# Kernel optimization log

Hardware: AMD Instinct MI355X
Metric: run time of the kernel (lower is better)

Reference implementation:

```python
import jax, jax.numpy as jnp
import numpy as np
import math

D_MODEL = 768
NUM_HEADS = 12
D_K = D_MODEL // NUM_HEADS

def setup_inputs() -> dict:
    key = jax.random.key(0)
    k_x, k_q, k_k, k_v, k_o = jax.random.split(key, 5)
    x = jax.random.normal(k_x, (2, 2048, D_MODEL), dtype=jnp.float32)
    std = math.sqrt(2.0 / (D_MODEL + D_MODEL))
    # trunc_normal approx: clip normal to [-3std, 3std]
    def tn(k):
        return jnp.clip(jax.random.normal(k, (D_MODEL, D_MODEL), dtype=jnp.float32) * std, -3 * std, 3 * std)
    return {
        "x": x,
        "weight_query": tn(k_q),
        "weight_key": tn(k_k),
        "weight_value": tn(k_v),
        "weight_output": tn(k_o),
    }

def reference(x, weight_query, weight_key, weight_value, weight_output):
    # x: (b, s, d_model); weights: (d_out, d_model)
    b, s, _ = x.shape
    def proj_heads(w):
        y = jnp.einsum('od,bsd->bso', w, x)  # (b, s, h*dk)
        return y.reshape(b, s, NUM_HEADS, D_K).transpose(0, 2, 1, 3)  # (b, h, s, dk)
    Q = proj_heads(weight_query)
    K = proj_heads(weight_key)
    V = proj_heads(weight_value)
    scores = jnp.einsum('bhqd,bhkd->bhqk', Q, K) / jnp.sqrt(jnp.asarray(D_K, x.dtype))
    causal = jnp.tril(jnp.ones((s, s), dtype=bool))  # (sq, sk)
    scores = jnp.where(causal, scores, -jnp.inf)
    attn = jax.nn.softmax(scores, axis=-1)
    out_heads = jnp.einsum('bhqk,bhkd->bhqd', attn, V)  # (b, h, s, dv)
    attn_out = out_heads.transpose(0, 2, 1, 3).reshape(b, s, NUM_HEADS * D_K)
    return jnp.einsum('di,bsi->bsd', weight_output, attn_out)
```

## Files before the change

### kernel.cpp

```cpp
#include <hip/hip_runtime.h>
#include <stdint.h>

typedef float f32x4 __attribute__((ext_vector_type(4)));
typedef __bf16 bf16x8 __attribute__((ext_vector_type(8)));
typedef uint32_t u32a  __attribute__((may_alias));
typedef uint2    u2a   __attribute__((may_alias));
typedef uint4    u4a   __attribute__((may_alias));

#define VS 2064

__device__ __forceinline__ ushort f2b(float f) {
  uint32_t u = __builtin_bit_cast(uint32_t, f);
  u += 0x7FFFu + ((u >> 16) & 1u);
  return (ushort)(u >> 16);
}
__device__ __forceinline__ uint32_t b16(uint32_t u) {
  u += 0x7FFFu + ((u >> 16) & 1u);
  return u >> 16;
}
__device__ __forceinline__ float blo(uint32_t a) {
  return __builtin_bit_cast(float, a << 16);
}
__device__ __forceinline__ float bhi(uint32_t a) {
  return __builtin_bit_cast(float, a & 0xFFFF0000u);
}

__device__ __forceinline__ bf16x8 ld_frag(const ushort* p) {
  u4a u = *(const u4a*)p;
  return __builtin_bit_cast(bf16x8, u);
}

__device__ __forceinline__ u4a cvt8(const float* p) {
  u4a a = *(const u4a*)p, b = *(const u4a*)(p + 4), o;
  o.x = b16(a.x) | (b16(a.y) << 16);
  o.y = b16(a.z) | (b16(a.w) << 16);
  o.z = b16(b.x) | (b16(b.y) << 16);
  o.w = b16(b.z) | (b16(b.w) << 16);
  return o;
}

__device__ __forceinline__ void load_lds16(const void* g, void* l) {
  __builtin_amdgcn_global_load_lds(
      (const __attribute__((address_space(1))) uint32_t*)g,
      (__attribute__((address_space(3))) uint32_t*)l, 16, 0, 0);
}

__global__ __launch_bounds__(256) void convert_kernel(
    const float* __restrict__ x,  const float* __restrict__ wq,
    const float* __restrict__ wk, const float* __restrict__ wv,
    const float* __restrict__ wo,
    ushort* __restrict__ xb,  ushort* __restrict__ wqb,
    ushort* __restrict__ wkb, ushort* __restrict__ wvb,
    ushort* __restrict__ wob)
{
  const size_t NX = 3145728, NW = 589824;
  size_t idx = ((size_t)blockIdx.x * 256 + threadIdx.x) * 8;
  const float* src; ushort* dst; size_t off;
  if      (idx < NX)          { src = x;  dst = xb;  off = idx; }
  else if (idx < NX + NW)     { src = wq; dst = wqb; off = idx - NX; }
  else if (idx < NX + 2 * NW) { src = wk; dst = wkb; off = idx - NX - NW; }
  else if (idx < NX + 3 * NW) { src = wv; dst = wvb; off = idx - NX - 2 * NW; }
  else                        { src = wo; dst = wob; off = idx - NX - 3 * NW; }
  *(u4a*)(dst + off) = cvt8(src + off);
}

__global__ __launch_bounds__(256) void gemm_qkv(
    const ushort* __restrict__ A,
    const ushort* __restrict__ B0, const ushort* __restrict__ B1,
    const ushort* __restrict__ B2,
    ushort* __restrict__ Qo, ushort* __restrict__ Ko, ushort* __restrict__ Vt,
    int M, int N, int K)
{
  const ushort* B = blockIdx.z == 0 ? B0 : (blockIdx.z == 1 ? B1 : B2);
  const int m0 = blockIdx.x * 128, n0 = blockIdx.y * 64;
  __shared__ ushort As[128 * 64];
  __shared__ ushort Bs[64 * 64];
  const int tid = threadIdx.x, wave = tid >> 6, lane = tid & 63;
  const int quad = lane >> 4, l16 = lane & 15;
  const int mw = (wave & 1) * 64, nw = (wave >> 1) * 32;
  f32x4 acc[4][2] = {};

  for (int k0 = 0; k0 < K; k0 += 64) {
#pragma unroll
    for (int i = 0; i < 4; ++i) {
      int c = i * 256 + tid;
      load_lds16(A + (size_t)(m0 + (c >> 3)) * K + k0 + (c & 7) * 8,
                 As + (size_t)(i * 256 + wave * 64) * 8);
    }
#pragma unroll
    for (int i = 0; i < 2; ++i) {
      int c = i * 256 + tid;
      load_lds16(B + (size_t)(n0 + (c >> 3)) * K + k0 + (c & 7) * 8,
                 Bs + (size_t)(i * 256 + wave * 64) * 8);
    }
    __syncthreads();
#pragma unroll
    for (int ks = 0; ks < 2; ++ks) {
      bf16x8 af[4], bfr[2];
#pragma unroll
      for (int i = 0; i < 4; ++i)
        af[i]  = ld_frag(As + (mw + i * 16 + l16) * 64 + ks * 32 + quad * 8);
#pragma unroll
      for (int j = 0; j < 2; ++j)
        bfr[j] = ld_frag(Bs + (nw + j * 16 + l16) * 64 + ks * 32 + quad * 8);
#pragma unroll
      for (int i = 0; i < 4; ++i)
#pragma unroll
        for (int j = 0; j < 2; ++j)
          acc[i][j] = __builtin_amdgcn_mfma_f32_16x16x32_bf16(af[i], bfr[j], acc[i][j], 0, 0, 0);
    }
    __syncthreads();
  }
  if (blockIdx.z < 2) {
    ushort* C = blockIdx.z == 0 ? Qo : Ko;
    const float sc = blockIdx.z == 0 ? 0.18033688f : 1.0f;
#pragma unroll
    for (int i = 0; i < 4; ++i)
#pragma unroll
      for (int j = 0; j < 2; ++j)
#pragma unroll
        for (int r = 0; r < 4; ++r) {
          int row = m0 + mw + i * 16 + quad * 4 + r;
          int col = n0 + nw + j * 16 + l16;
          C[(size_t)row * N + col] = f2b(acc[i][j][r] * sc);
        }
  } else {
#pragma unroll
    for (int i = 0; i < 4; ++i)
#pragma unroll
      for (int j = 0; j < 2; ++j) {
        int col = n0 + nw + j * 16 + l16;
        int h = col >> 6, dv = col & 63;
        int t = m0 + mw + i * 16 + quad * 4;
        int b = t >> 11, s = t & 2047;
        u2a pw;
        pw.x = (uint32_t)f2b(acc[i][j][0]) | ((uint32_t)f2b(acc[i][j][1]) << 16);
        pw.y = (uint32_t)f2b(acc[i][j][2]) | ((uint32_t)f2b(acc[i][j][3]) << 16);
        *(u2a*)(Vt + (((size_t)b * 12 + h) * 64 + dv) * VS + s) = pw;
      }
  }
}

__global__ __launch_bounds__(256) void gemm_out(
    const ushort* __restrict__ A, const ushort* __restrict__ B,
    float* __restrict__ C, int M, int N, int K)
{
  const int m0 = blockIdx.x * 64, n0 = blockIdx.y * 64;
  __shared__ ushort As[64 * 64];
  __shared__ ushort Bs[64 * 64];
  const int tid = threadIdx.x, wave = tid >> 6, lane = tid & 63;
  const int quad = lane >> 4, l16 = lane & 15;
  const int mw = (wave & 1) * 32, nw = (wave >> 1) * 32;
  f32x4 acc[2][2] = {};

  for (int k0 = 0; k0 < K; k0 += 64) {
#pragma unroll
    for (int i = 0; i < 2; ++i) {
      int c = i * 256 + tid;
      load_lds16(A + (size_t)(m0 + (c >> 3)) * K + k0 + (c & 7) * 8,
                 As + (size_t)(i * 256 + wave * 64) * 8);
      load_lds16(B + (size_t)(n0 + (c >> 3)) * K + k0 + (c & 7) * 8,
                 Bs + (size_t)(i * 256 + wave * 64) * 8);
    }
    __syncthreads();
#pragma unroll
    for (int ks = 0; ks < 2; ++ks) {
      bf16x8 af[2], bfr[2];
#pragma unroll
      for (int i = 0; i < 2; ++i)
        af[i]  = ld_frag(As + (mw + i * 16 + l16) * 64 + ks * 32 + quad * 8);
#pragma unroll
      for (int j = 0; j < 2; ++j)
        bfr[j] = ld_frag(Bs + (nw + j * 16 + l16) * 64 + ks * 32 + quad * 8);
#pragma unroll
      for (int i = 0; i < 2; ++i)
#pragma unroll
        for (int j = 0; j < 2; ++j)
          acc[i][j] = __builtin_amdgcn_mfma_f32_16x16x32_bf16(af[i], bfr[j], acc[i][j], 0, 0, 0);
    }
    __syncthreads();
  }
#pragma unroll
  for (int i = 0; i < 2; ++i)
#pragma unroll
    for (int j = 0; j < 2; ++j)
#pragma unroll
      for (int r = 0; r < 4; ++r) {
        int row = m0 + mw + i * 16 + quad * 4 + r;
        int col = n0 + nw + j * 16 + l16;
        C[(size_t)row * N + col] = acc[i][j][r];
      }
}

__global__ __launch_bounds__(256) void attn_kernel(
    const ushort* __restrict__ Qb, const ushort* __restrict__ Kb,
    const ushort* __restrict__ Vt, ushort* __restrict__ Opart,
    float* __restrict__ Lp)
{
  const int S = 2048, DM = 768;
  const int pair = blockIdx.x >> 2, j = blockIdx.x & 3;
  const int h = blockIdx.y, bb = blockIdx.z;
  const ushort* Qp  = Qb + (size_t)bb * S * DM + h * 64;
  const ushort* Kp  = Kb + (size_t)bb * S * DM + h * 64;
  const ushort* Vth = Vt + ((size_t)bb * 12 + h) * 64 * VS;

  __shared__ ushort Ks[64 * 72];
  __shared__ ushort Vs[64 * 72];

  const int tid = threadIdx.x, wave = tid >> 6, lane = tid & 63;
  const int quad = lane >> 4, l16 = lane & 15;
  const float NEG_BIG = -1.0e30f;

  const int qtA = pair, qtB = 31 - pair;
  const int qgA = qtA * 64 + wave * 16 + l16;
  const int qgB = qtB * 64 + wave * 16 + l16;

  bf16x8 bqA0 = ld_frag(Qp + (size_t)qgA * DM + quad * 8);
  bf16x8 bqA1 = ld_frag(Qp + (size_t)qgA * DM + 32 + quad * 8);
  bf16x8 bqB0 = ld_frag(Qp + (size_t)qgB * DM + quad * 8);
  bf16x8 bqB1 = ld_frag(Qp + (size_t)qgB * DM + 32 + quad * 8);

  u4a one4; one4.x = one4.y = one4.z = one4.w = 0x3F803F80u;
  const bf16x8 ones = __builtin_bit_cast(bf16x8, one4);

  f32x4 accA[4] = {}, accB[4] = {};
  f32x4 alA = {}, alB = {};

  for (int kt = j; kt <= qtB; kt += 4) {
    const int kk0 = kt * 64;
#pragma unroll
    for (int i = 0; i < 2; ++i) {
      int c = i * 256 + tid;
      int r = c >> 3, col = (c & 7) * 8;
      *(u4a*)(Ks + r * 72 + col) = *(const u4a*)(Kp + (size_t)(kk0 + r) * DM + col);
    }
#pragma unroll
    for (int i = 0; i < 2; ++i) {
      int c = i * 256 + tid;
      int dv = c >> 3, kc8 = c & 7;
      u4a g = *(const u4a*)(Vth + (size_t)dv * VS + kk0 + kc8 * 8);
      int pos = ((kc8 >> 2) * 32) + ((kc8 & 1) * 16) + (((kc8 >> 1) & 1) * 4);
      u2a lo, hi;
      lo.x = g.x; lo.y = g.y; hi.x = g.z; hi.y = g.w;
      *(u2a*)(Vs + dv * 72 + pos)     = lo;
      *(u2a*)(Vs + dv * 72 + pos + 8) = hi;
    }
    __syncthreads();

    auto strip = [&](const bf16x8& bq0, const bf16x8& bq1, f32x4* acc_o,
                     f32x4& acc_l, int qg, bool domask) {
      f32x4 sacc[4] = {};
#pragma unroll
      for (int tt = 0; tt < 4; ++tt) {
        bf16x8 ak0 = ld_frag(Ks + (tt * 16 + l16) * 72 + quad * 8);
        bf16x8 ak1 = ld_frag(Ks + (tt * 16 + l16) * 72 + 32 + quad * 8);
        sacc[tt] = __builtin_amdgcn_mfma_f32_16x16x32_bf16(ak0, bq0, sacc[tt], 0, 0, 0);
        sacc[tt] = __builtin_amdgcn_mfma_f32_16x16x32_bf16(ak1, bq1, sacc[tt], 0, 0, 0);
      }
      if (domask) {
#pragma unroll
        for (int tt = 0; tt < 4; ++tt)
#pragma unroll
          for (int r = 0; r < 4; ++r) {
            int kkg = kk0 + tt * 16 + quad * 4 + r;
            if (kkg > qg) sacc[tt][r] = NEG_BIG;
          }
      }
#pragma unroll
      for (int g = 0; g < 2; ++g) {
        u4a pu;
        {
          int tt = g * 2;
          uint32_t u0 = __builtin_bit_cast(uint32_t, exp2f(sacc[tt][0]));
          uint32_t u1 = __builtin_bit_cast(uint32_t, exp2f(sacc[tt][1]));
          uint32_t u2 = __builtin_bit_cast(uint32_t, exp2f(sacc[tt][2]));
          uint32_t u3 = __builtin_bit_cast(uint32_t, exp2f(sacc[tt][3]));
          pu.x = __builtin_amdgcn_perm(u1, u0, 0x07060302u);
          pu.y = __builtin_amdgcn_perm(u3, u2, 0x07060302u);
          u0 = __builtin_bit_cast(uint32_t, exp2f(sacc[tt + 1][0]));
          u1 = __builtin_bit_cast(uint32_t, exp2f(sacc[tt + 1][1]));
          u2 = __builtin_bit_cast(uint32_t, exp2f(sacc[tt + 1][2]));
          u3 = __builtin_bit_cast(uint32_t, exp2f(sacc[tt + 1][3]));
          pu.z = __builtin_amdgcn_perm(u1, u0, 0x07060302u);
          pu.w = __builtin_amdgcn_perm(u3, u2, 0x07060302u);
        }
        bf16x8 ap = __builtin_bit_cast(bf16x8, pu);
        acc_l = __builtin_amdgcn_mfma_f32_16x16x32_bf16(ap, ones, acc_l, 0, 0, 0);
#pragma unroll
        for (int ct = 0; ct < 4; ++ct) {
          bf16x8 bv = ld_frag(Vs + (size_t)(ct * 16 + l16) * 72 + g * 32 + quad * 8);
          acc_o[ct] = __builtin_amdgcn_mfma_f32_16x16x32_bf16(ap, bv, acc_o[ct], 0, 0, 0);
        }
      }
    };

    strip(bqB0, bqB1, accB, alB, qgB, kt == qtB);
    if (kt <= qtA)
      strip(bqA0, bqA1, accA, alA, qgA, kt == qtA);
    __syncthreads();
  }

  const int base = ((bb * 12 + h) << 5);
  const int r0 = wave * 16 + quad * 4;
  {
    const int slot = (base + qtB) * 4 + j;
    ushort* Os = Opart + (size_t)slot * 4096;
#pragma unroll
    for (int ct = 0; ct < 4; ++ct) {
      int col = ct * 16 + l16;
      Os[(r0 + 0) * 64 + col] = f2b(accB[ct][0]);
      Os[(r0 + 1) * 64 + col] = f2b(accB[ct][1]);
      Os[(r0 + 2) * 64 + col] = f2b(accB[ct][2]);
      Os[(r0 + 3) * 64 + col] = f2b(accB[ct][3]);
    }
    if (l16 == 0) {
#pragma unroll
      for (int r = 0; r < 4; ++r)
        Lp[(size_t)slot * 64 + r0 + r] = alB[r];
    }
  }
  {
    const int slot = (base + qtA) * 4 + j;
    ushort* Os = Opart + (size_t)slot * 4096;
#pragma unroll
    for (int ct = 0; ct < 4; ++ct) {
      int col = ct * 16 + l16;
      Os[(r0 + 0) * 64 + col] = f2b(accA[ct][0]);
      Os[(r0 + 1) * 64 + col] = f2b(accA[ct][1]);
      Os[(r0 + 2) * 64 + col] = f2b(accA[ct][2]);
      Os[(r0 + 3) * 64 + col] = f2b(accA[ct][3]);
    }
    if (l16 == 0) {
#pragma unroll
      for (int r = 0; r < 4; ++r)
        Lp[(size_t)slot * 64 + r0 + r] = alA[r];
    }
  }
}

__global__ __launch_bounds__(256) void combine_kernel(
    const ushort* __restrict__ Opart, const float* __restrict__ Lp,
    ushort* __restrict__ Ab, int split)
{
  const int sid = blockIdx.x;
  const int bb = sid / 384, rem = sid % 384, h = rem >> 5, qt = rem & 31;
  const int t = threadIdx.x, row = t >> 2, cg = (t & 3) * 16;
  const float* lp = Lp + (size_t)sid * split * 64 + row;
  float denom = 0.0f;
  for (int i = 0; i < split; ++i) denom += lp[(size_t)i * 64];
  const float inv = 1.0f / denom;
  float os[16] = {};
  const ushort* p0 = Opart + (size_t)sid * split * 4096 + row * 64 + cg;
  for (int i = 0; i < split; ++i) {
#pragma unroll
    for (int g = 0; g < 2; ++g) {
      u4a a = *(const u4a*)(p0 + (size_t)i * 4096 + g * 8);
      os[g * 8 + 0] += blo(a.x); os[g * 8 + 1] += bhi(a.x);
      os[g * 8 + 2] += blo(a.y); os[g * 8 + 3] += bhi(a.y);
      os[g * 8 + 4] += blo(a.z); os[g * 8 + 5] += bhi(a.z);
      os[g * 8 + 6] += blo(a.w); os[g * 8 + 7] += bhi(a.w);
    }
  }
  ushort* dst = Ab + ((size_t)(bb * 2048 + qt * 64 + row)) * 768 + h * 64 + cg;
#pragma unroll
  for (int g = 0; g < 2; ++g) {
    u4a o;
    o.x = (uint32_t)f2b(os[g * 8 + 0] * inv) | ((uint32_t)f2b(os[g * 8 + 1] * inv) << 16);
    o.y = (uint32_t)f2b(os[g * 8 + 2] * inv) | ((uint32_t)f2b(os[g * 8 + 3] * inv) << 16);
    o.z = (uint32_t)f2b(os[g * 8 + 4] * inv) | ((uint32_t)f2b(os[g * 8 + 5] * inv) << 16);
    o.w = (uint32_t)f2b(os[g * 8 + 6] * inv) | ((uint32_t)f2b(os[g * 8 + 7] * inv) << 16);
    *(u4a*)(dst + g * 8) = o;
  }
}

extern "C" void kernel_launch(void* const* d_in, const int* in_sizes, int n_in,
                              void* d_out, int out_size, void* d_ws, size_t ws_size,
                              hipStream_t stream) {
  (void)in_sizes; (void)n_in; (void)out_size; (void)ws_size;
  const float* x  = (const float*)d_in[0];
  const float* wq = (const float*)d_in[1];
  const float* wk = (const float*)d_in[2];
  const float* wv = (const float*)d_in[3];
  const float* wo = (const float*)d_in[4];

  const size_t NT = (size_t)4096 * 768;
  const size_t NW = (size_t)768 * 768;
  const size_t NV = (size_t)24 * 64 * VS;
  ushort* xb    = (ushort*)d_ws;
  ushort* Qbuf  = xb + NT;
  ushort* Kbuf  = Qbuf + NT;
  ushort* Vt    = Kbuf + NT;
  ushort* wqb   = Vt + NV;
  ushort* wkb   = wqb + NW;
  ushort* wvb   = wkb + NW;
  ushort* wob   = wvb + NW;
  ushort* Opart = wob + NW;
  float* Lp     = (float*)(Opart + (size_t)3072 * 4096);
  ushort* Abuf  = xb;

  convert_kernel<<<2688, 256, 0, stream>>>(x, wq, wk, wv, wo,
                                           xb, wqb, wkb, wvb, wob);
  gemm_qkv<<<dim3(32, 12, 3), 256, 0, stream>>>(
      xb, wqb, wkb, wvb, Qbuf, Kbuf, Vt, 4096, 768, 768);
  attn_kernel<<<dim3(64, 12, 2), 256, 0, stream>>>(Qbuf, Kbuf, Vt, Opart, Lp);
  combine_kernel<<<768, 256, 0, stream>>>(Opart, Lp, Abuf, 4);
  gemm_out<<<dim3(64, 12), 256, 0, stream>>>(
      Abuf, wob, (float*)d_out, 4096, 768, 768);
}
```

Baseline: 161.0 us.

## Double-buffer K/V tiles in attention and halve the key-split factor

Adds register-staged prefetch of the next K/V tile into a second shared-memory buffer, so global loads overlap with the MFMA work on the current tile, leaving one barrier per iteration. The key dimension split per query-tile pair drops from 4 to 2, which halves the attention grid, the partial output buffers and the combine work. In exchange each block runs a longer serial loop, there are fewer blocks to fill the GPU, and shared memory and register use go up.

```diff
diff --git a/kernel.cpp b/kernel.cpp
--- a/kernel.cpp
+++ b/kernel.cpp
@@ -198,14 +198,14 @@
     float* __restrict__ Lp)
 {
   const int S = 2048, DM = 768;
-  const int pair = blockIdx.x >> 2, j = blockIdx.x & 3;
+  const int pair = blockIdx.x >> 1, j = blockIdx.x & 1;
   const int h = blockIdx.y, bb = blockIdx.z;
   const ushort* Qp  = Qb + (size_t)bb * S * DM + h * 64;
   const ushort* Kp  = Kb + (size_t)bb * S * DM + h * 64;
   const ushort* Vth = Vt + ((size_t)bb * 12 + h) * 64 * VS;
 
-  __shared__ ushort Ks[64 * 72];
-  __shared__ ushort Vs[64 * 72];
+  __shared__ ushort Ks[2][64 * 72];
+  __shared__ ushort Vs[2][64 * 72];
 
   const int tid = threadIdx.x, wave = tid >> 6, lane = tid & 63;
   const int quad = lane >> 4, l16 = lane & 15;
@@ -226,34 +226,57 @@
   f32x4 accA[4] = {}, accB[4] = {};
   f32x4 alA = {}, alB = {};
 
-  for (int kt = j; kt <= qtB; kt += 4) {
-    const int kk0 = kt * 64;
+  u4a kr[2], vr[2];
+
+  {
+    const int kk0 = j * 64;
 #pragma unroll
     for (int i = 0; i < 2; ++i) {
       int c = i * 256 + tid;
-      int r = c >> 3, col = (c & 7) * 8;
-      *(u4a*)(Ks + r * 72 + col) = *(const u4a*)(Kp + (size_t)(kk0 + r) * DM + col);
+      kr[i] = *(const u4a*)(Kp + (size_t)(kk0 + (c >> 3)) * DM + (c & 7) * 8);
+      vr[i] = *(const u4a*)(Vth + (size_t)(c >> 3) * VS + kk0 + (c & 7) * 8);
     }
 #pragma unroll
     for (int i = 0; i < 2; ++i) {
       int c = i * 256 + tid;
+      *(u4a*)(&Ks[0][(c >> 3) * 72 + (c & 7) * 8]) = kr[i];
       int dv = c >> 3, kc8 = c & 7;
-      u4a g = *(const u4a*)(Vth + (size_t)dv * VS + kk0 + kc8 * 8);
       int pos = ((kc8 >> 2) * 32) + ((kc8 & 1) * 16) + (((kc8 >> 1) & 1) * 4);
       u2a lo, hi;
-      lo.x = g.x; lo.y = g.y; hi.x = g.z; hi.y = g.w;
-      *(u2a*)(Vs + dv * 72 + pos)     = lo;
-      *(u2a*)(Vs + dv * 72 + pos + 8) = hi;
-    }
-    __syncthreads();
+      lo.x = kr[0].x;
+      (void)lo;
+      u2a vlo, vhi;
+      vlo.x = vr[i].x; vlo.y = vr[i].y; vhi.x = vr[i].z; vhi.y = vr[i].w;
+      *(u2a*)(&Vs[0][dv * 72 + pos])     = vlo;
+      *(u2a*)(&Vs[0][dv * 72 + pos + 8]) = vhi;
+    }
+  }
+  __syncthreads();
+
+  int cur = 0;
+  for (int kt = j; kt <= qtB; kt += 2) {
+    const int kk0 = kt * 64;
+    const int nx = kt + 2;
+    const bool hasNext = (nx <= qtB);
+    if (hasNext) {
+      const int nk0 = nx * 64;
+#pragma unroll
+      for (int i = 0; i < 2; ++i) {
+        int c = i * 256 + tid;
+        kr[i] = *(const u4a*)(Kp + (size_t)(nk0 + (c >> 3)) * DM + (c & 7) * 8);
+        vr[i] = *(const u4a*)(Vth + (size_t)(c >> 3) * VS + nk0 + (c & 7) * 8);
+      }
+    }
+    const ushort* Kc = &Ks[cur][0];
+    const ushort* Vc = &Vs[cur][0];
 
     auto strip = [&](const bf16x8& bq0, const bf16x8& bq1, f32x4* acc_o,
                      f32x4& acc_l, int qg, bool domask) {
       f32x4 sacc[4] = {};
 #pragma unroll
       for (int tt = 0; tt < 4; ++tt) {
-        bf16x8 ak0 = ld_frag(Ks + (tt * 16 + l16) * 72 + quad * 8);
-        bf16x8 ak1 = ld_frag(Ks + (tt * 16 + l16) * 72 + 32 + quad * 8);
+        bf16x8 ak0 = ld_frag(Kc + (tt * 16 + l16) * 72 + quad * 8);
+        bf16x8 ak1 = ld_frag(Kc + (tt * 16 + l16) * 72 + 32 + quad * 8);
         sacc[tt] = __builtin_amdgcn_mfma_f32_16x16x32_bf16(ak0, bq0, sacc[tt], 0, 0, 0);
         sacc[tt] = __builtin_amdgcn_mfma_f32_16x16x32_bf16(ak1, bq1, sacc[tt], 0, 0, 0);
       }
@@ -288,7 +311,7 @@
         acc_l = __builtin_amdgcn_mfma_f32_16x16x32_bf16(ap, ones, acc_l, 0, 0, 0);
 #pragma unroll
         for (int ct = 0; ct < 4; ++ct) {
-          bf16x8 bv = ld_frag(Vs + (size_t)(ct * 16 + l16) * 72 + g * 32 + quad * 8);
+          bf16x8 bv = ld_frag(Vc + (size_t)(ct * 16 + l16) * 72 + g * 32 + quad * 8);
           acc_o[ct] = __builtin_amdgcn_mfma_f32_16x16x32_bf16(ap, bv, acc_o[ct], 0, 0, 0);
         }
       }
@@ -297,13 +320,30 @@
     strip(bqB0, bqB1, accB, alB, qgB, kt == qtB);
     if (kt <= qtA)
       strip(bqA0, bqA1, accA, alA, qgA, kt == qtA);
+
+    if (hasNext) {
+      ushort* Kn = &Ks[cur ^ 1][0];
+      ushort* Vn = &Vs[cur ^ 1][0];
+#pragma unroll
+      for (int i = 0; i < 2; ++i) {
+        int c = i * 256 + tid;
+        *(u4a*)(&Kn[(c >> 3) * 72 + (c & 7) * 8]) = kr[i];
+        int dv = c >> 3, kc8 = c & 7;
+        int pos = ((kc8 >> 2) * 32) + ((kc8 & 1) * 16) + (((kc8 >> 1) & 1) * 4);
+        u2a vlo, vhi;
+        vlo.x = vr[i].x; vlo.y = vr[i].y; vhi.x = vr[i].z; vhi.y = vr[i].w;
+        *(u2a*)(&Vn[dv * 72 + pos])     = vlo;
+        *(u2a*)(&Vn[dv * 72 + pos + 8]) = vhi;
+      }
+    }
     __syncthreads();
+    cur ^= 1;
   }
 
   const int base = ((bb * 12 + h) << 5);
   const int r0 = wave * 16 + quad * 4;
   {
-    const int slot = (base + qtB) * 4 + j;
+    const int slot = (base + qtB) * 2 + j;
     ushort* Os = Opart + (size_t)slot * 4096;
 #pragma unroll
     for (int ct = 0; ct < 4; ++ct) {
@@ -320,7 +360,7 @@
     }
   }
   {
-    const int slot = (base + qtA) * 4 + j;
+    const int slot = (base + qtA) * 2 + j;
     ushort* Os = Opart + (size_t)slot * 4096;
 #pragma unroll
     for (int ct = 0; ct < 4; ++ct) {
@@ -395,15 +435,15 @@
   ushort* wvb   = wkb + NW;
   ushort* wob   = wvb + NW;
   ushort* Opart = wob + NW;
-  float* Lp     = (float*)(Opart + (size_t)3072 * 4096);
+  float* Lp     = (float*)(Opart + (size_t)1536 * 4096);
   ushort* Abuf  = xb;
 
   convert_kernel<<<2688, 256, 0, stream>>>(x, wq, wk, wv, wo,
                                            xb, wqb, wkb, wvb, wob);
   gemm_qkv<<<dim3(32, 12, 3), 256, 0, stream>>>(
       xb, wqb, wkb, wvb, Qbuf, Kbuf, Vt, 4096, 768, 768);
-  attn_kernel<<<dim3(64, 12, 2), 256, 0, stream>>>(Qbuf, Kbuf, Vt, Opart, Lp);
-  combine_kernel<<<768, 256, 0, stream>>>(Opart, Lp, Abuf, 4);
+  attn_kernel<<<dim3(32, 12, 2), 256, 0, stream>>>(Qbuf, Kbuf, Vt, Opart, Lp);
+  combine_kernel<<<768, 256, 0, stream>>>(Opart, Lp, Abuf, 2);
   gemm_out<<<dim3(64, 12), 256, 0, stream>>>(
       Abuf, wob, (float*)d_out, 4096, 768, 768);
 }
```

Result: slower. 178.6 us (+11.0%).
